# Kernel optimization log

Measured on AMD Instinct MI355X. Metric: run time of the kernel, lower is better.

The kernel has to match this reference:

```python
import jax, jax.numpy as jnp
import numpy as np

K = 16  # neighbors
EPS = 1e-3  # Keras BatchNormalization default epsilon


def _bn(x, gamma, beta, mean, var):
    return (x - mean) * jax.lax.rsqrt(var + EPS) * gamma + beta


def setup_inputs() -> dict:
    key = jax.random.key(0)
    ks = jax.random.split(key, 16)
    B, P, C = 128, 256, 64
    inp = {
        "points": jax.random.normal(ks[0], (B, P, 3), jnp.float32),
        "features": jax.random.normal(ks[1], (B, P, C), jnp.float32),
        "w0": jax.random.normal(ks[2], (2 * C, 64), jnp.float32) * 0.08,
        "w1": jax.random.normal(ks[3], (64, 64), jnp.float32) * 0.12,
        "w2": jax.random.normal(ks[4], (64, 64), jnp.float32) * 0.12,
        "gammas": 0.8 + 0.4 * jax.random.uniform(ks[5], (3, 64), jnp.float32),
        "betas": 0.1 * jax.random.normal(ks[6], (3, 64), jnp.float32),
        "means": 0.1 * jax.random.normal(ks[7], (3, 64), jnp.float32),
        "variances": 0.5 + jax.random.uniform(ks[8], (3, 64), jnp.float32),
        "sc_w": jax.random.normal(ks[9], (C, 64), jnp.float32) * 0.12,
        "sc_gamma": 0.8 + 0.4 * jax.random.uniform(ks[10], (64,), jnp.float32),
        "sc_beta": 0.1 * jax.random.normal(ks[11], (64,), jnp.float32),
        "sc_mean": 0.1 * jax.random.normal(ks[12], (64,), jnp.float32),
        "sc_var": 0.5 + jax.random.uniform(ks[13], (64,), jnp.float32),
    }
    return inp


def reference(points, features, w0, w1, w2, gammas, betas, means, variances,
              sc_w, sc_gamma, sc_beta, sc_mean, sc_var):
    B, P, C = features.shape
    # pairwise squared-distance matrix: ||a||^2 - 2 a.b + ||b||^2  -> [B, P, P]
    r = jnp.sum(points * points, axis=2, keepdims=True)  # [B, P, 1]
    m = jnp.einsum('bpc,bqc->bpq', points, points)
    d = r - 2.0 * m + jnp.swapaxes(r, 1, 2)
    # top_k of -d: K+1 nearest (incl. self at position 0), drop self
    _, idx = jax.lax.top_k(-d, K + 1)
    idx = idx[:, :, 1:]  # [B, P, K]
    # KNN gather of features
    knn_fts = features[jnp.arange(B)[:, None, None], idx]  # [B, P, K, C]
    center = jnp.broadcast_to(features[:, :, None, :], (B, P, K, C))
    x = jnp.concatenate([center, knn_fts - center], axis=-1)  # [B, P, K, 2C]
    # per-edge MLP: 1x1 conv + BN (inference) + relu
    for i, w in enumerate((w0, w1, w2)):
        x = jnp.einsum('bpkc,cd->bpkd', x, w)
        x = _bn(x, gammas[i], betas[i], means[i], variances[i])
        x = jax.nn.relu(x)
    fts = jnp.mean(x, axis=2)  # average pooling over neighbors -> [B, P, 64]
    # shortcut 1x1 conv + BN
    sc = jnp.einsum('bpc,cd->bpd', features, sc_w)
    sc = _bn(sc, sc_gamma, sc_beta, sc_mean, sc_var)
    return jax.nn.relu(sc + fts)
```

## Files before the change

kernel.cpp:

```cpp
#include <hip/hip_runtime.h>
#include <math.h>

#define NBATCH 128
#define NP 256
#define NC 64
#define KNN 16
#define EPSV 1e-3f

typedef __bf16 bf16_t;
typedef bf16_t bf16x8 __attribute__((ext_vector_type(8)));
typedef float f32x4 __attribute__((ext_vector_type(4)));
typedef unsigned short u16x4 __attribute__((ext_vector_type(4)));

static __device__ __forceinline__ f32x4 mfma16(bf16x8 a, bf16x8 b, f32x4 c) {
    return __builtin_amdgcn_mfma_f32_16x16x32_bf16(a, b, c, 0, 0, 0);
}
static __device__ __forceinline__ unsigned short f2bfu(float f) {
    union { bf16_t b; unsigned short u; } cv; cv.b = (bf16_t)f; return cv.u;
}
static __device__ __forceinline__ float bfu2f(unsigned short u) {
    unsigned x = ((unsigned)u) << 16;
    return __int_as_float((int)x);
}
static __device__ __forceinline__ unsigned umin2(unsigned a, unsigned b) { return a < b ? a : b; }
static __device__ __forceinline__ unsigned umax2(unsigned a, unsigned b) { return a > b ? a : b; }

static __device__ __forceinline__ bf16x8 packrelu(f32x4 a, f32x4 b) {
    bf16x8 r;
    r[0] = (bf16_t)fmaxf(a[0], 0.f); r[1] = (bf16_t)fmaxf(a[1], 0.f);
    r[2] = (bf16_t)fmaxf(a[2], 0.f); r[3] = (bf16_t)fmaxf(a[3], 0.f);
    r[4] = (bf16_t)fmaxf(b[0], 0.f); r[5] = (bf16_t)fmaxf(b[1], 0.f);
    r[6] = (bf16_t)fmaxf(b[2], 0.f); r[7] = (bf16_t)fmaxf(b[3], 0.f);
    return r;
}

template <int CTRL>
static __device__ __forceinline__ float dppadd(float v) {
    int x = __builtin_amdgcn_mov_dpp(__float_as_int(v), CTRL, 0xF, 0xF, true);
    return v + __int_as_float(x);
}
static __device__ __forceinline__ float sum16(float v) {
    v = dppadd<0xB1>(v);
    v = dppadd<0x4E>(v);
    v = dppadd<0x141>(v);
    v = dppadd<0x140>(v);
    return v;
}

#define CFENCE() asm volatile("" ::: "memory")

#define INSERTK(k_)                                                   \
    do {                                                              \
        _Pragma("unroll")                                             \
        for (int ii = KNN - 1; ii >= 1; --ii)                         \
            bk[ii] = umin2(umax2((k_), bk[ii - 1]), bk[ii]);          \
        bk[0] = umin2((k_), bk[0]);                                   \
    } while (0)

__global__ __launch_bounds__(256) void setup_kernel(
    const float* __restrict__ points, const float* __restrict__ features,
    const float* __restrict__ w0, const float* __restrict__ w1,
    const float* __restrict__ w2, const float* __restrict__ sc_w,
    const float* __restrict__ gammas, const float* __restrict__ betas,
    const float* __restrict__ means, const float* __restrict__ variances,
    const float* __restrict__ sc_gamma, const float* __restrict__ sc_beta,
    const float* __restrict__ sc_mean, const float* __restrict__ sc_var,
    unsigned short* __restrict__ fbf, unsigned short* __restrict__ wsf,
    float* __restrict__ bnp, int* __restrict__ knn_out)
{
    const int bid = blockIdx.x;
    if (bid < 1024) {
        const int tid = bid * 256 + threadIdx.x;
        const float4 a = ((const float4*)features)[tid * 2];
        const float4 b = ((const float4*)features)[tid * 2 + 1];
        union { unsigned short s[8]; uint4 v; } r;
        r.s[0] = f2bfu(a.x); r.s[1] = f2bfu(a.y); r.s[2] = f2bfu(a.z); r.s[3] = f2bfu(a.w);
        r.s[4] = f2bfu(b.x); r.s[5] = f2bfu(b.y); r.s[6] = f2bfu(b.z); r.s[7] = f2bfu(b.w);
        ((uint4*)fbf)[tid] = r.v;
    } else if (bid < 1106) {
        const int tid = (bid - 1024) * 256 + threadIdx.x;
        if (tid < 20480) {
            const int region = tid >> 12;
            const int e2 = tid & 4095;
            const int f = e2 >> 9;
            const int r = e2 & 511;
            const int lane = r >> 3, j = r & 7;
            const int ks = f >> 2, t = f & 3;
            const int m = lane & 15;
            const int k_in = ks * 32 + (lane >> 4) * 8 + j;
            const int kp = (t >> 1) * 32 + (m >> 2) * 8 + (t & 1) * 4 + (m & 3);
            float v;
            if (region == 0)      v = w0[k_in * 64 + kp] - w0[(64 + k_in) * 64 + kp];
            else if (region == 1) v = w0[(64 + k_in) * 64 + kp];
            else if (region == 2) {
                float s1 = gammas[k_in] * rsqrtf(variances[k_in] + EPSV);
                v = s1 * w1[k_in * 64 + kp];
            } else if (region == 3) {
                float s2 = gammas[64 + k_in] * rsqrtf(variances[64 + k_in] + EPSV);
                v = s2 * w2[k_in * 64 + kp];
            } else {
                v = sc_w[k_in * 64 + (4 * m + t)];
            }
            wsf[tid] = f2bfu(v);
        } else {
            const int e = tid - 20480;
            if (e < 192) {
                const int L = e >> 6;
                const int pos = e & 63;
                const int t = pos >> 4, m = pos & 15;
                const int c = (t >> 1) * 32 + (m >> 2) * 8 + (t & 1) * 4 + (m & 3);
                float scl = gammas[L * 64 + c] * rsqrtf(variances[L * 64 + c] + EPSV);
                float shf = betas[L * 64 + c] - means[L * 64 + c] * scl;
                bnp[e] = shf / scl;
            } else if (e < 256) {
                const int c = e - 192;
                float s3 = gammas[128 + c] * rsqrtf(variances[128 + c] + EPSV);
                bnp[e] = s3 * (1.f / 16.f);
            } else if (e < 320) {
                const int c = e - 256;
                bnp[e] = sc_gamma[c] * rsqrtf(sc_var[c] + EPSV);
            } else if (e < 384) {
                const int c = e - 320;
                float s = sc_gamma[c] * rsqrtf(sc_var[c] + EPSV);
                bnp[e] = sc_beta[c] - sc_mean[c] * s;
            }
        }
    } else {
        __shared__ __align__(16) float4 sp[NP];
        __shared__ unsigned sk[128][17];
        const int kb = bid - 1106;
        const int bb = kb >> 1;
        const int qbase = (kb & 1) * 128;
        const int t = threadIdx.x;
        const int qt = t & 127;
        const int half = t >> 7;
        const int p = qbase + qt;

        const float* pb = points + (size_t)bb * NP * 3;
        sp[t] = make_float4(pb[t * 3 + 0], pb[t * 3 + 1], pb[t * 3 + 2], 0.f);
        __syncthreads();

        const float4 qp = sp[p];
        unsigned bk[KNN];
#pragma unroll
        for (int i = 0; i < KNN; ++i) bk[i] = 0xFFFFFFFFu;

        const int cbase = half * 128;
#pragma unroll 4
        for (int c = 0; c < 128; ++c) {
            const int cand = cbase + c;
            const float4 P = sp[cand];
            const float dx = qp.x - P.x, dy = qp.y - P.y, dz = qp.z - P.z;
            const float d = fmaf(dx, dx, fmaf(dy, dy, dz * dz));
            unsigned key = (__float_as_uint(d) & 0xFFFFFF00u) | (unsigned)cand;
            key = (cand == p) ? 0xFFFFFFFFu : key;
            INSERTK(key);
        }

        if (half == 1) {
#pragma unroll
            for (int i = 0; i < KNN; ++i) sk[qt][i] = bk[i];
        }
        __syncthreads();
        if (half == 0) {
            for (int j = 0; j < KNN; ++j) {
                const unsigned key = sk[qt][j];
                if (key >= bk[KNN - 1]) break;
                INSERTK(key);
            }
            int* op = knn_out + ((size_t)bb * NP + p) * KNN;
#pragma unroll
            for (int i = 0; i < KNN; ++i) op[i] = (int)(bk[i] & 0xFFu);
        }
    }
}

__global__ __launch_bounds__(256) void edge_kernel(
    const unsigned short* __restrict__ fbf, const int* __restrict__ knn_idx,
    const unsigned short* __restrict__ wsf, const float* __restrict__ bnp,
    float* __restrict__ out)
{
    __shared__ __align__(16) float s0buf[4][8][64];
    __shared__ __align__(16) unsigned short ftsbuf[4][8][64];

    const int tid = threadIdx.x;
    const int wid = tid >> 6;
    const int l = tid & 63;
    const int i = l & 15;
    const int h = l >> 4;
    const int wg = (blockIdx.x & 7) * 128 + (blockIdx.x >> 3);
    const int p0 = (wg * 4 + wid) * 8;
    const int b = p0 >> 8;

    bf16x8 wr[24];
    {
        const bf16x8* __restrict__ W = (const bf16x8*)(wsf + 4096);
#pragma unroll
        for (int f = 0; f < 24; ++f) wr[f] = W[f * 64 + l];
    }
    #define WF(fi_) (wr[fi_])

    f32x4 cin2[4], cin3[4];
#pragma unroll
    for (int t = 0; t < 4; ++t) {
        cin2[t] = *(const f32x4*)&bnp[64 + t * 16 + 4 * h];
        cin3[t] = *(const f32x4*)&bnp[128 + t * 16 + 4 * h];
    }

    {
        const bf16x8* __restrict__ WV = (const bf16x8*)(wsf);
        const unsigned short* cp = fbf + (size_t)(p0 + (i & 7)) * NC;
        bf16x8 b0 = *(const bf16x8*)(cp + 8 * h);
        bf16x8 b1 = *(const bf16x8*)(cp + 32 + 8 * h);
#pragma unroll
        for (int t = 0; t < 4; ++t) {
            f32x4 acc = *(const f32x4*)&bnp[t * 16 + 4 * h];
            acc = mfma16(WV[t * 64 + l], b0, acc);
            acc = mfma16(WV[(4 + t) * 64 + l], b1, acc);
            if (i < 8)
                *(f32x4*)&s0buf[wid][i][t * 16 + 4 * h] = acc;
        }
    }
    int nks[8];
#pragma unroll
    for (int q = 0; q < 8; ++q) nks[q] = knn_idx[(size_t)(p0 + q) * KNN + i];
    CFENCE();

    bf16x8 fb0, fb1;
    {
        const unsigned short* sp = fbf + (size_t)(b * NP + nks[0]) * NC;
        fb0 = *(const bf16x8*)(sp + 8 * h);
        fb1 = *(const bf16x8*)(sp + 32 + 8 * h);
    }

#pragma unroll
    for (int q = 0; q < 8; ++q) {
        f32x4 acc[4];
#pragma unroll
        for (int t = 0; t < 4; ++t) {
            f32x4 z = *(const f32x4*)&s0buf[wid][q][t * 16 + 4 * h];
            z = mfma16(WF(t), fb0, z);
            acc[t] = mfma16(WF(4 + t), fb1, z);
        }
        bf16x8 g0, g1;
        if (q < 7) {
            const unsigned short* sp = fbf + (size_t)(b * NP + nks[(q + 1) & 7]) * NC;
            g0 = *(const bf16x8*)(sp + 8 * h);
            g1 = *(const bf16x8*)(sp + 32 + 8 * h);
        }
        bf16x8 x0 = packrelu(acc[0], acc[1]);
        bf16x8 x1 = packrelu(acc[2], acc[3]);

#pragma unroll
        for (int t = 0; t < 4; ++t) {
            f32x4 z = mfma16(WF(8 + t), x0, cin2[t]);
            acc[t] = mfma16(WF(12 + t), x1, z);
        }
        bf16x8 y0 = packrelu(acc[0], acc[1]);
        bf16x8 y1 = packrelu(acc[2], acc[3]);

#pragma unroll
        for (int t = 0; t < 4; ++t) {
            f32x4 z = mfma16(WF(16 + t), y0, cin3[t]);
            acc[t] = mfma16(WF(20 + t), y1, z);
        }
        float st[4][4];
#pragma unroll
        for (int t = 0; t < 4; ++t)
#pragma unroll
            for (int r = 0; r < 4; ++r)
                st[t][r] = sum16(fmaxf(acc[t][r], 0.f));
        if (i == 0) {
#pragma unroll
            for (int t = 0; t < 4; ++t) {
                u16x4 pk;
#pragma unroll
                for (int r = 0; r < 4; ++r) pk[r] = f2bfu(st[t][r]);
                *(u16x4*)&ftsbuf[wid][q][(t >> 1) * 32 + h * 8 + (t & 1) * 4] = pk;
            }
        }
        fb0 = g0; fb1 = g1;
    }
    CFENCE();

    {
        const bf16x8* __restrict__ WS = (const bf16x8*)(wsf + 16384);
        const int i4 = 4 * i;
        float4 sscl = *(const float4*)&bnp[256 + i4];
        float4 sshf = *(const float4*)&bnp[320 + i4];
        float4 f3q  = *(const float4*)&bnp[192 + i4];
        const unsigned short* fp = fbf + (size_t)(p0 + (i & 7)) * NC;
        bf16x8 a0 = *(const bf16x8*)(fp + 8 * h);
        bf16x8 a1 = *(const bf16x8*)(fp + 32 + 8 * h);
        f32x4 acc[4];
#pragma unroll
        for (int t = 0; t < 4; ++t) {
            f32x4 z = {0.f, 0.f, 0.f, 0.f};
            z = mfma16(a0, WS[t * 64 + l], z);
            acc[t] = mfma16(a1, WS[(4 + t) * 64 + l], z);
        }
        if (h < 2) {
            const float* ss_ = (const float*)&sscl;
            const float* sf_ = (const float*)&sshf;
            const float* f3_ = (const float*)&f3q;
#pragma unroll
            for (int r = 0; r < 4; ++r) {
                const int q = h * 4 + r;
                u16x4 ftsu = *(const u16x4*)&ftsbuf[wid][q][i4];
                float4 o;
                float* o_ = (float*)&o;
#pragma unroll
                for (int t = 0; t < 4; ++t)
                    o_[t] = fmaxf(fmaf(acc[t][r], ss_[t], sf_[t]) + bfu2f(ftsu[t]) * f3_[t], 0.f);
                *(float4*)&out[(size_t)(p0 + q) * NC + i4] = o;
            }
        }
    }
    #undef WF
}

extern "C" void kernel_launch(void* const* d_in, const int* in_sizes, int n_in,
                              void* d_out, int out_size, void* d_ws, size_t ws_size,
                              hipStream_t stream) {
    const float* points    = (const float*)d_in[0];
    const float* features  = (const float*)d_in[1];
    const float* w0        = (const float*)d_in[2];
    const float* w1        = (const float*)d_in[3];
    const float* w2        = (const float*)d_in[4];
    const float* gammas    = (const float*)d_in[5];
    const float* betas     = (const float*)d_in[6];
    const float* means     = (const float*)d_in[7];
    const float* variances = (const float*)d_in[8];
    const float* sc_w      = (const float*)d_in[9];
    const float* sc_gamma  = (const float*)d_in[10];
    const float* sc_beta   = (const float*)d_in[11];
    const float* sc_mean   = (const float*)d_in[12];
    const float* sc_var    = (const float*)d_in[13];
    float* out = (float*)d_out;

    int* knn_buf = (int*)d_ws;
    unsigned short* fbf = (unsigned short*)((char*)d_ws + (1 << 21));
    unsigned short* wsf = (unsigned short*)((char*)d_ws + (3 << 21));
    float* bnp = (float*)((char*)d_ws + (3 << 21) + 40960);

    setup_kernel<<<1362, 256, 0, stream>>>(points, features, w0, w1, w2, sc_w,
                                           gammas, betas, means, variances,
                                           sc_gamma, sc_beta, sc_mean, sc_var,
                                           fbf, wsf, bnp, knn_buf);
    edge_kernel<<<NBATCH * NP / 32, 256, 0, stream>>>(fbf, knn_buf, wsf, bnp, out);
}
```

Before: 50.39 us.

## Fuse KNN, feature conversion and edge MLP into one per-batch kernel

Merges the KNN search, the bf16 feature conversion and the edge MLP into a single kernel. Each block handles half a batch and stages that batch's bf16 features in swizzled LDS, so neighbour gathers read LDS instead of global memory and the knn indices and bf16 feature buffer never go to global memory. Weight and BN preparation stays in a small separate kernel. The trade-off is a grid of only 256 blocks with large LDS use (about 50KB), which lowers occupancy and parallelism. The KNN phase also keeps the same half-idle merge step as before, and each block converts all 256 rows of its batch, so every batch is converted twice.

```diff
diff --git a/kernel.cpp b/kernel.cpp
--- a/kernel.cpp
+++ b/kernel.cpp
@@ -57,94 +57,108 @@
         bk[0] = umin2((k_), bk[0]);                                   \
     } while (0)
 
-__global__ __launch_bounds__(256) void setup_kernel(
-    const float* __restrict__ points, const float* __restrict__ features,
+__global__ __launch_bounds__(256) void prep_kernel(
     const float* __restrict__ w0, const float* __restrict__ w1,
     const float* __restrict__ w2, const float* __restrict__ sc_w,
     const float* __restrict__ gammas, const float* __restrict__ betas,
     const float* __restrict__ means, const float* __restrict__ variances,
     const float* __restrict__ sc_gamma, const float* __restrict__ sc_beta,
     const float* __restrict__ sc_mean, const float* __restrict__ sc_var,
-    unsigned short* __restrict__ fbf, unsigned short* __restrict__ wsf,
-    float* __restrict__ bnp, int* __restrict__ knn_out)
+    unsigned short* __restrict__ wsf, float* __restrict__ bnp)
 {
-    const int bid = blockIdx.x;
-    if (bid < 1024) {
-        const int tid = bid * 256 + threadIdx.x;
-        const float4 a = ((const float4*)features)[tid * 2];
-        const float4 b = ((const float4*)features)[tid * 2 + 1];
-        union { unsigned short s[8]; uint4 v; } r;
-        r.s[0] = f2bfu(a.x); r.s[1] = f2bfu(a.y); r.s[2] = f2bfu(a.z); r.s[3] = f2bfu(a.w);
-        r.s[4] = f2bfu(b.x); r.s[5] = f2bfu(b.y); r.s[6] = f2bfu(b.z); r.s[7] = f2bfu(b.w);
-        ((uint4*)fbf)[tid] = r.v;
-    } else if (bid < 1106) {
-        const int tid = (bid - 1024) * 256 + threadIdx.x;
-        if (tid < 20480) {
-            const int region = tid >> 12;
-            const int e2 = tid & 4095;
-            const int f = e2 >> 9;
-            const int r = e2 & 511;
-            const int lane = r >> 3, j = r & 7;
-            const int ks = f >> 2, t = f & 3;
-            const int m = lane & 15;
-            const int k_in = ks * 32 + (lane >> 4) * 8 + j;
-            const int kp = (t >> 1) * 32 + (m >> 2) * 8 + (t & 1) * 4 + (m & 3);
-            float v;
-            if (region == 0)      v = w0[k_in * 64 + kp] - w0[(64 + k_in) * 64 + kp];
-            else if (region == 1) v = w0[(64 + k_in) * 64 + kp];
-            else if (region == 2) {
-                float s1 = gammas[k_in] * rsqrtf(variances[k_in] + EPSV);
-                v = s1 * w1[k_in * 64 + kp];
-            } else if (region == 3) {
-                float s2 = gammas[64 + k_in] * rsqrtf(variances[64 + k_in] + EPSV);
-                v = s2 * w2[k_in * 64 + kp];
-            } else {
-                v = sc_w[k_in * 64 + (4 * m + t)];
-            }
-            wsf[tid] = f2bfu(v);
+    const int tid = blockIdx.x * 256 + threadIdx.x;
+    if (tid < 20480) {
+        const int region = tid >> 12;
+        const int e2 = tid & 4095;
+        const int f = e2 >> 9;
+        const int r = e2 & 511;
+        const int lane = r >> 3, j = r & 7;
+        const int ks = f >> 2, t = f & 3;
+        const int m = lane & 15;
+        const int k_in = ks * 32 + (lane >> 4) * 8 + j;
+        const int kp = (t >> 1) * 32 + (m >> 2) * 8 + (t & 1) * 4 + (m & 3);
+        float v;
+        if (region == 0)      v = w0[k_in * 64 + kp] - w0[(64 + k_in) * 64 + kp];
+        else if (region == 1) v = w0[(64 + k_in) * 64 + kp];
+        else if (region == 2) {
+            float s1 = gammas[k_in] * rsqrtf(variances[k_in] + EPSV);
+            v = s1 * w1[k_in * 64 + kp];
+        } else if (region == 3) {
+            float s2 = gammas[64 + k_in] * rsqrtf(variances[64 + k_in] + EPSV);
+            v = s2 * w2[k_in * 64 + kp];
         } else {
-            const int e = tid - 20480;
-            if (e < 192) {
-                const int L = e >> 6;
-                const int pos = e & 63;
-                const int t = pos >> 4, m = pos & 15;
-                const int c = (t >> 1) * 32 + (m >> 2) * 8 + (t & 1) * 4 + (m & 3);
-                float scl = gammas[L * 64 + c] * rsqrtf(variances[L * 64 + c] + EPSV);
-                float shf = betas[L * 64 + c] - means[L * 64 + c] * scl;
-                bnp[e] = shf / scl;
-            } else if (e < 256) {
-                const int c = e - 192;
-                float s3 = gammas[128 + c] * rsqrtf(variances[128 + c] + EPSV);
-                bnp[e] = s3 * (1.f / 16.f);
-            } else if (e < 320) {
-                const int c = e - 256;
-                bnp[e] = sc_gamma[c] * rsqrtf(sc_var[c] + EPSV);
-            } else if (e < 384) {
-                const int c = e - 320;
-                float s = sc_gamma[c] * rsqrtf(sc_var[c] + EPSV);
-                bnp[e] = sc_beta[c] - sc_mean[c] * s;
-            }
-        }
+            v = sc_w[k_in * 64 + (4 * m + t)];
+        }
+        wsf[tid] = f2bfu(v);
     } else {
-        __shared__ __align__(16) float4 sp[NP];
-        __shared__ unsigned sk[128][17];
-        const int kb = bid - 1106;
-        const int bb = kb >> 1;
-        const int qbase = (kb & 1) * 128;
-        const int t = threadIdx.x;
+        const int e = tid - 20480;
+        if (e < 192) {
+            const int L = e >> 6;
+            const int pos = e & 63;
+            const int t = pos >> 4, m = pos & 15;
+            const int c = (t >> 1) * 32 + (m >> 2) * 8 + (t & 1) * 4 + (m & 3);
+            float scl = gammas[L * 64 + c] * rsqrtf(variances[L * 64 + c] + EPSV);
+            float shf = betas[L * 64 + c] - means[L * 64 + c] * scl;
+            bnp[e] = shf / scl;
+        } else if (e < 256) {
+            const int c = e - 192;
+            float s3 = gammas[128 + c] * rsqrtf(variances[128 + c] + EPSV);
+            bnp[e] = s3 * (1.f / 16.f);
+        } else if (e < 320) {
+            const int c = e - 256;
+            bnp[e] = sc_gamma[c] * rsqrtf(sc_var[c] + EPSV);
+        } else if (e < 384) {
+            const int c = e - 320;
+            float s = sc_gamma[c] * rsqrtf(sc_var[c] + EPSV);
+            bnp[e] = sc_beta[c] - sc_mean[c] * s;
+        }
+    }
+}
+
+__global__ __launch_bounds__(256) void mega_kernel(
+    const float* __restrict__ points, const float* __restrict__ features,
+    const unsigned short* __restrict__ wsf, const float* __restrict__ bnp,
+    float* __restrict__ out)
+{
+    __shared__ __align__(16) unsigned short fLDS[NP * NC];
+    __shared__ __align__(16) float4 sp[NP];
+    __shared__ unsigned sk[128][17];
+    __shared__ unsigned short nkbuf[128][16];
+    __shared__ __align__(16) float s0buf[4][8][64];
+    __shared__ __align__(16) unsigned short ftsbuf[4][8][64];
+
+    const int kb = blockIdx.x;
+    const int bb = kb >> 1;
+    const int qbase = (kb & 1) * 128;
+    const int t = threadIdx.x;
+
+    {
+        const float* pb = points + (size_t)bb * NP * 3;
+        sp[t] = make_float4(pb[t * 3 + 0], pb[t * 3 + 1], pb[t * 3 + 2], 0.f);
+        const float* fb = features + (size_t)bb * NP * NC;
+#pragma unroll
+        for (int cc = 0; cc < 8; ++cc) {
+            const int c = t + cc * 256;
+            const int row = c >> 3, ch8 = c & 7;
+            const float4 a = *(const float4*)&fb[row * NC + ch8 * 8];
+            const float4 b2 = *(const float4*)&fb[row * NC + ch8 * 8 + 4];
+            union { unsigned short s[8]; uint4 v; } r;
+            r.s[0] = f2bfu(a.x); r.s[1] = f2bfu(a.y); r.s[2] = f2bfu(a.z); r.s[3] = f2bfu(a.w);
+            r.s[4] = f2bfu(b2.x); r.s[5] = f2bfu(b2.y); r.s[6] = f2bfu(b2.z); r.s[7] = f2bfu(b2.w);
+            const int sc = ch8 ^ (row & 7);
+            *(uint4*)&fLDS[row * NC + sc * 8] = r.v;
+        }
+    }
+    __syncthreads();
+
+    {
         const int qt = t & 127;
         const int half = t >> 7;
         const int p = qbase + qt;
-
-        const float* pb = points + (size_t)bb * NP * 3;
-        sp[t] = make_float4(pb[t * 3 + 0], pb[t * 3 + 1], pb[t * 3 + 2], 0.f);
-        __syncthreads();
-
         const float4 qp = sp[p];
         unsigned bk[KNN];
 #pragma unroll
-        for (int i = 0; i < KNN; ++i) bk[i] = 0xFFFFFFFFu;
-
+        for (int ii = 0; ii < KNN; ++ii) bk[ii] = 0xFFFFFFFFu;
         const int cbase = half * 128;
 #pragma unroll 4
         for (int c = 0; c < 128; ++c) {
@@ -156,10 +170,9 @@
             key = (cand == p) ? 0xFFFFFFFFu : key;
             INSERTK(key);
         }
-
         if (half == 1) {
 #pragma unroll
-            for (int i = 0; i < KNN; ++i) sk[qt][i] = bk[i];
+            for (int ii = 0; ii < KNN; ++ii) sk[qt][ii] = bk[ii];
         }
         __syncthreads();
         if (half == 0) {
@@ -168,29 +181,17 @@
                 if (key >= bk[KNN - 1]) break;
                 INSERTK(key);
             }
-            int* op = knn_out + ((size_t)bb * NP + p) * KNN;
-#pragma unroll
-            for (int i = 0; i < KNN; ++i) op[i] = (int)(bk[i] & 0xFFu);
-        }
-    }
-}
-
-__global__ __launch_bounds__(256) void edge_kernel(
-    const unsigned short* __restrict__ fbf, const int* __restrict__ knn_idx,
-    const unsigned short* __restrict__ wsf, const float* __restrict__ bnp,
-    float* __restrict__ out)
-{
-    __shared__ __align__(16) float s0buf[4][8][64];
-    __shared__ __align__(16) unsigned short ftsbuf[4][8][64];
-
-    const int tid = threadIdx.x;
-    const int wid = tid >> 6;
-    const int l = tid & 63;
+#pragma unroll
+            for (int ii = 0; ii < KNN; ++ii)
+                nkbuf[qt][ii] = (unsigned short)(bk[ii] & 0xFFu);
+        }
+    }
+    __syncthreads();
+
+    const int wid = t >> 6;
+    const int l = t & 63;
     const int i = l & 15;
     const int h = l >> 4;
-    const int wg = (blockIdx.x & 7) * 128 + (blockIdx.x >> 3);
-    const int p0 = (wg * 4 + wid) * 8;
-    const int b = p0 >> 8;
 
     bf16x8 wr[24];
     {
@@ -198,125 +199,128 @@
 #pragma unroll
         for (int f = 0; f < 24; ++f) wr[f] = W[f * 64 + l];
     }
-    #define WF(fi_) (wr[fi_])
-
     f32x4 cin2[4], cin3[4];
 #pragma unroll
-    for (int t = 0; t < 4; ++t) {
-        cin2[t] = *(const f32x4*)&bnp[64 + t * 16 + 4 * h];
-        cin3[t] = *(const f32x4*)&bnp[128 + t * 16 + 4 * h];
-    }
-
-    {
-        const bf16x8* __restrict__ WV = (const bf16x8*)(wsf);
-        const unsigned short* cp = fbf + (size_t)(p0 + (i & 7)) * NC;
-        bf16x8 b0 = *(const bf16x8*)(cp + 8 * h);
-        bf16x8 b1 = *(const bf16x8*)(cp + 32 + 8 * h);
-#pragma unroll
-        for (int t = 0; t < 4; ++t) {
-            f32x4 acc = *(const f32x4*)&bnp[t * 16 + 4 * h];
-            acc = mfma16(WV[t * 64 + l], b0, acc);
-            acc = mfma16(WV[(4 + t) * 64 + l], b1, acc);
-            if (i < 8)
-                *(f32x4*)&s0buf[wid][i][t * 16 + 4 * h] = acc;
-        }
-    }
-    int nks[8];
-#pragma unroll
-    for (int q = 0; q < 8; ++q) nks[q] = knn_idx[(size_t)(p0 + q) * KNN + i];
-    CFENCE();
-
-    bf16x8 fb0, fb1;
-    {
-        const unsigned short* sp = fbf + (size_t)(b * NP + nks[0]) * NC;
-        fb0 = *(const bf16x8*)(sp + 8 * h);
-        fb1 = *(const bf16x8*)(sp + 32 + 8 * h);
-    }
-
-#pragma unroll
-    for (int q = 0; q < 8; ++q) {
-        f32x4 acc[4];
-#pragma unroll
-        for (int t = 0; t < 4; ++t) {
-            f32x4 z = *(const f32x4*)&s0buf[wid][q][t * 16 + 4 * h];
-            z = mfma16(WF(t), fb0, z);
-            acc[t] = mfma16(WF(4 + t), fb1, z);
-        }
-        bf16x8 g0, g1;
-        if (q < 7) {
-            const unsigned short* sp = fbf + (size_t)(b * NP + nks[(q + 1) & 7]) * NC;
-            g0 = *(const bf16x8*)(sp + 8 * h);
-            g1 = *(const bf16x8*)(sp + 32 + 8 * h);
-        }
-        bf16x8 x0 = packrelu(acc[0], acc[1]);
-        bf16x8 x1 = packrelu(acc[2], acc[3]);
-
-#pragma unroll
-        for (int t = 0; t < 4; ++t) {
-            f32x4 z = mfma16(WF(8 + t), x0, cin2[t]);
-            acc[t] = mfma16(WF(12 + t), x1, z);
-        }
-        bf16x8 y0 = packrelu(acc[0], acc[1]);
-        bf16x8 y1 = packrelu(acc[2], acc[3]);
-
-#pragma unroll
-        for (int t = 0; t < 4; ++t) {
-            f32x4 z = mfma16(WF(16 + t), y0, cin3[t]);
-            acc[t] = mfma16(WF(20 + t), y1, z);
-        }
-        float st[4][4];
-#pragma unroll
-        for (int t = 0; t < 4; ++t)
-#pragma unroll
-            for (int r = 0; r < 4; ++r)
-                st[t][r] = sum16(fmaxf(acc[t][r], 0.f));
-        if (i == 0) {
-#pragma unroll
-            for (int t = 0; t < 4; ++t) {
-                u16x4 pk;
-#pragma unroll
-                for (int r = 0; r < 4; ++r) pk[r] = f2bfu(st[t][r]);
-                *(u16x4*)&ftsbuf[wid][q][(t >> 1) * 32 + h * 8 + (t & 1) * 4] = pk;
-            }
-        }
-        fb0 = g0; fb1 = g1;
-    }
-    CFENCE();
-
-    {
-        const bf16x8* __restrict__ WS = (const bf16x8*)(wsf + 16384);
-        const int i4 = 4 * i;
-        float4 sscl = *(const float4*)&bnp[256 + i4];
-        float4 sshf = *(const float4*)&bnp[320 + i4];
-        float4 f3q  = *(const float4*)&bnp[192 + i4];
-        const unsigned short* fp = fbf + (size_t)(p0 + (i & 7)) * NC;
-        bf16x8 a0 = *(const bf16x8*)(fp + 8 * h);
-        bf16x8 a1 = *(const bf16x8*)(fp + 32 + 8 * h);
-        f32x4 acc[4];
-#pragma unroll
-        for (int t = 0; t < 4; ++t) {
-            f32x4 z = {0.f, 0.f, 0.f, 0.f};
-            z = mfma16(a0, WS[t * 64 + l], z);
-            acc[t] = mfma16(a1, WS[(4 + t) * 64 + l], z);
-        }
-        if (h < 2) {
-            const float* ss_ = (const float*)&sscl;
-            const float* sf_ = (const float*)&sshf;
-            const float* f3_ = (const float*)&f3q;
-#pragma unroll
-            for (int r = 0; r < 4; ++r) {
-                const int q = h * 4 + r;
-                u16x4 ftsu = *(const u16x4*)&ftsbuf[wid][q][i4];
-                float4 o;
-                float* o_ = (float*)&o;
-#pragma unroll
-                for (int t = 0; t < 4; ++t)
-                    o_[t] = fmaxf(fmaf(acc[t][r], ss_[t], sf_[t]) + bfu2f(ftsu[t]) * f3_[t], 0.f);
-                *(float4*)&out[(size_t)(p0 + q) * NC + i4] = o;
-            }
-        }
-    }
-    #undef WF
+    for (int tq = 0; tq < 4; ++tq) {
+        cin2[tq] = *(const f32x4*)&bnp[64 + tq * 16 + 4 * h];
+        cin3[tq] = *(const f32x4*)&bnp[128 + tq * 16 + 4 * h];
+    }
+
+    const bf16x8* __restrict__ WV = (const bf16x8*)(wsf);
+    const bf16x8* __restrict__ WS = (const bf16x8*)(wsf + 16384);
+
+    for (int seg = 0; seg < 4; ++seg) {
+        const int qr0 = seg * 32 + wid * 8;
+
+        {
+            const int crow = qbase + qr0 + (i & 7);
+            const int swl = crow & 7;
+            bf16x8 b0 = *(const bf16x8*)&fLDS[crow * NC + (h ^ swl) * 8];
+            bf16x8 b1 = *(const bf16x8*)&fLDS[crow * NC + ((4 + h) ^ swl) * 8];
+#pragma unroll
+            for (int tq = 0; tq < 4; ++tq) {
+                f32x4 acc = *(const f32x4*)&bnp[tq * 16 + 4 * h];
+                acc = mfma16(WV[tq * 64 + l], b0, acc);
+                acc = mfma16(WV[(4 + tq) * 64 + l], b1, acc);
+                if (i < 8)
+                    *(f32x4*)&s0buf[wid][i][tq * 16 + 4 * h] = acc;
+            }
+        }
+        int nks[8];
+#pragma unroll
+        for (int q = 0; q < 8; ++q) nks[q] = nkbuf[qr0 + q][i];
+        CFENCE();
+
+        bf16x8 fb0, fb1;
+        {
+            const int nk = nks[0], swn = nk & 7;
+            fb0 = *(const bf16x8*)&fLDS[nk * NC + (h ^ swn) * 8];
+            fb1 = *(const bf16x8*)&fLDS[nk * NC + ((4 + h) ^ swn) * 8];
+        }
+
+#pragma unroll
+        for (int q = 0; q < 8; ++q) {
+            f32x4 acc[4];
+#pragma unroll
+            for (int tq = 0; tq < 4; ++tq) {
+                f32x4 z = *(const f32x4*)&s0buf[wid][q][tq * 16 + 4 * h];
+                z = mfma16(wr[tq], fb0, z);
+                acc[tq] = mfma16(wr[4 + tq], fb1, z);
+            }
+            bf16x8 g0, g1;
+            if (q < 7) {
+                const int nk = nks[q + 1], swn = nk & 7;
+                g0 = *(const bf16x8*)&fLDS[nk * NC + (h ^ swn) * 8];
+                g1 = *(const bf16x8*)&fLDS[nk * NC + ((4 + h) ^ swn) * 8];
+            }
+            bf16x8 x0 = packrelu(acc[0], acc[1]);
+            bf16x8 x1 = packrelu(acc[2], acc[3]);
+#pragma unroll
+            for (int tq = 0; tq < 4; ++tq) {
+                f32x4 z = mfma16(wr[8 + tq], x0, cin2[tq]);
+                acc[tq] = mfma16(wr[12 + tq], x1, z);
+            }
+            bf16x8 y0 = packrelu(acc[0], acc[1]);
+            bf16x8 y1 = packrelu(acc[2], acc[3]);
+#pragma unroll
+            for (int tq = 0; tq < 4; ++tq) {
+                f32x4 z = mfma16(wr[16 + tq], y0, cin3[tq]);
+                acc[tq] = mfma16(wr[20 + tq], y1, z);
+            }
+            float st[4][4];
+#pragma unroll
+            for (int tq = 0; tq < 4; ++tq)
+#pragma unroll
+                for (int r = 0; r < 4; ++r)
+                    st[tq][r] = sum16(fmaxf(acc[tq][r], 0.f));
+            if (i == 0) {
+#pragma unroll
+                for (int tq = 0; tq < 4; ++tq) {
+                    u16x4 pk;
+#pragma unroll
+                    for (int r = 0; r < 4; ++r) pk[r] = f2bfu(st[tq][r]);
+                    *(u16x4*)&ftsbuf[wid][q][(tq >> 1) * 32 + h * 8 + (tq & 1) * 4] = pk;
+                }
+            }
+            fb0 = g0; fb1 = g1;
+        }
+        CFENCE();
+
+        {
+            const int i4 = 4 * i;
+            float4 sscl = *(const float4*)&bnp[256 + i4];
+            float4 sshf = *(const float4*)&bnp[320 + i4];
+            float4 f3q  = *(const float4*)&bnp[192 + i4];
+            const int crow = qbase + qr0 + (i & 7);
+            const int swl = crow & 7;
+            bf16x8 a0 = *(const bf16x8*)&fLDS[crow * NC + (h ^ swl) * 8];
+            bf16x8 a1 = *(const bf16x8*)&fLDS[crow * NC + ((4 + h) ^ swl) * 8];
+            f32x4 acc[4];
+#pragma unroll
+            for (int tq = 0; tq < 4; ++tq) {
+                f32x4 z = {0.f, 0.f, 0.f, 0.f};
+                z = mfma16(a0, WS[tq * 64 + l], z);
+                acc[tq] = mfma16(a1, WS[(4 + tq) * 64 + l], z);
+            }
+            if (h < 2) {
+                const float* ss_ = (const float*)&sscl;
+                const float* sf_ = (const float*)&sshf;
+                const float* f3_ = (const float*)&f3q;
+#pragma unroll
+                for (int r = 0; r < 4; ++r) {
+                    const int q = h * 4 + r;
+                    u16x4 ftsu = *(const u16x4*)&ftsbuf[wid][q][i4];
+                    float4 o;
+                    float* o_ = (float*)&o;
+#pragma unroll
+                    for (int tq = 0; tq < 4; ++tq)
+                        o_[tq] = fmaxf(fmaf(acc[tq][r], ss_[tq], sf_[tq]) + bfu2f(ftsu[tq]) * f3_[tq], 0.f);
+                    *(float4*)&out[(size_t)(bb * NP + qbase + qr0 + q) * NC + i4] = o;
+                }
+            }
+        }
+        CFENCE();
+    }
 }
 
 extern "C" void kernel_launch(void* const* d_in, const int* in_sizes, int n_in,
@@ -338,14 +342,11 @@
     const float* sc_var    = (const float*)d_in[13];
     float* out = (float*)d_out;
 
-    int* knn_buf = (int*)d_ws;
-    unsigned short* fbf = (unsigned short*)((char*)d_ws + (1 << 21));
-    unsigned short* wsf = (unsigned short*)((char*)d_ws + (3 << 21));
-    float* bnp = (float*)((char*)d_ws + (3 << 21) + 40960);
-
-    setup_kernel<<<1362, 256, 0, stream>>>(points, features, w0, w1, w2, sc_w,
-                                           gammas, betas, means, variances,
-                                           sc_gamma, sc_beta, sc_mean, sc_var,
-                                           fbf, wsf, bnp, knn_buf);
-    edge_kernel<<<NBATCH * NP / 32, 256, 0, stream>>>(fbf, knn_buf, wsf, bnp, out);
-}
+    unsigned short* wsf = (unsigned short*)d_ws;
+    float* bnp = (float*)((char*)d_ws + 40960);
+
+    prep_kernel<<<82, 256, 0, stream>>>(w0, w1, w2, sc_w, gammas, betas, means,
+                                        variances, sc_gamma, sc_beta, sc_mean,
+                                        sc_var, wsf, bnp);
+    mega_kernel<<<NBATCH * 2, 256, 0, stream>>>(points, features, wsf, bnp, out);
+}
```

Result: slower. 51.80 us (+2.8%).

## Transpose layer-3 MFMA so neighbor sum uses two cross-half shuffles

Applied to the files above, without the earlier changes.

Layer 3 now swaps the MFMA operands so the output puts the neighbor dimension across the four accumulator registers and the 16-lane halves. The neighbor pooling becomes an in-register add plus two xor-shuffles, replacing sixteen 4-step DPP reductions. Pooled features stay in fp32 in shared memory instead of bf16. The w2 and shortcut weights and the BN bias layout are reordered to match, and the center-feature loads are reused for the shortcut. The tradeoffs are scalar 4-byte output stores in place of float4 stores, and a larger shared buffer.

```diff
diff --git a/kernel.cpp b/kernel.cpp
--- a/kernel.cpp
+++ b/kernel.cpp
@@ -10,17 +10,12 @@
 typedef __bf16 bf16_t;
 typedef bf16_t bf16x8 __attribute__((ext_vector_type(8)));
 typedef float f32x4 __attribute__((ext_vector_type(4)));
-typedef unsigned short u16x4 __attribute__((ext_vector_type(4)));
 
 static __device__ __forceinline__ f32x4 mfma16(bf16x8 a, bf16x8 b, f32x4 c) {
     return __builtin_amdgcn_mfma_f32_16x16x32_bf16(a, b, c, 0, 0, 0);
 }
 static __device__ __forceinline__ unsigned short f2bfu(float f) {
     union { bf16_t b; unsigned short u; } cv; cv.b = (bf16_t)f; return cv.u;
-}
-static __device__ __forceinline__ float bfu2f(unsigned short u) {
-    unsigned x = ((unsigned)u) << 16;
-    return __int_as_float((int)x);
 }
 static __device__ __forceinline__ unsigned umin2(unsigned a, unsigned b) { return a < b ? a : b; }
 static __device__ __forceinline__ unsigned umax2(unsigned a, unsigned b) { return a > b ? a : b; }
@@ -32,19 +27,6 @@
     r[4] = (bf16_t)fmaxf(b[0], 0.f); r[5] = (bf16_t)fmaxf(b[1], 0.f);
     r[6] = (bf16_t)fmaxf(b[2], 0.f); r[7] = (bf16_t)fmaxf(b[3], 0.f);
     return r;
-}
-
-template <int CTRL>
-static __device__ __forceinline__ float dppadd(float v) {
-    int x = __builtin_amdgcn_mov_dpp(__float_as_int(v), CTRL, 0xF, 0xF, true);
-    return v + __int_as_float(x);
-}
-static __device__ __forceinline__ float sum16(float v) {
-    v = dppadd<0xB1>(v);
-    v = dppadd<0x4E>(v);
-    v = dppadd<0x141>(v);
-    v = dppadd<0x140>(v);
-    return v;
 }
 
 #define CFENCE() asm volatile("" ::: "memory")
@@ -88,29 +70,39 @@
             const int ks = f >> 2, t = f & 3;
             const int m = lane & 15;
             const int k_in = ks * 32 + (lane >> 4) * 8 + j;
-            const int kp = (t >> 1) * 32 + (m >> 2) * 8 + (t & 1) * 4 + (m & 3);
             float v;
-            if (region == 0)      v = w0[k_in * 64 + kp] - w0[(64 + k_in) * 64 + kp];
-            else if (region == 1) v = w0[(64 + k_in) * 64 + kp];
-            else if (region == 2) {
-                float s1 = gammas[k_in] * rsqrtf(variances[k_in] + EPSV);
-                v = s1 * w1[k_in * 64 + kp];
-            } else if (region == 3) {
-                float s2 = gammas[64 + k_in] * rsqrtf(variances[64 + k_in] + EPSV);
-                v = s2 * w2[k_in * 64 + kp];
+            if (region <= 2) {
+                const int kp = (t >> 1) * 32 + (m >> 2) * 8 + (t & 1) * 4 + (m & 3);
+                if (region == 0)      v = w0[k_in * 64 + kp] - w0[(64 + k_in) * 64 + kp];
+                else if (region == 1) v = w0[(64 + k_in) * 64 + kp];
+                else {
+                    float s1 = gammas[k_in] * rsqrtf(variances[k_in] + EPSV);
+                    v = s1 * w1[k_in * 64 + kp];
+                }
             } else {
-                v = sc_w[k_in * 64 + (4 * m + t)];
+                const int col = t * 16 + m;
+                if (region == 3) {
+                    float s2 = gammas[64 + k_in] * rsqrtf(variances[64 + k_in] + EPSV);
+                    v = s2 * w2[k_in * 64 + col];
+                } else {
+                    v = sc_w[k_in * 64 + col];
+                }
             }
             wsf[tid] = f2bfu(v);
         } else {
             const int e = tid - 20480;
-            if (e < 192) {
+            if (e < 128) {
                 const int L = e >> 6;
                 const int pos = e & 63;
                 const int t = pos >> 4, m = pos & 15;
                 const int c = (t >> 1) * 32 + (m >> 2) * 8 + (t & 1) * 4 + (m & 3);
                 float scl = gammas[L * 64 + c] * rsqrtf(variances[L * 64 + c] + EPSV);
                 float shf = betas[L * 64 + c] - means[L * 64 + c] * scl;
+                bnp[e] = shf / scl;
+            } else if (e < 192) {
+                const int c = e - 128;
+                float scl = gammas[128 + c] * rsqrtf(variances[128 + c] + EPSV);
+                float shf = betas[128 + c] - means[128 + c] * scl;
                 bnp[e] = shf / scl;
             } else if (e < 256) {
                 const int c = e - 192;
@@ -181,7 +173,7 @@
     float* __restrict__ out)
 {
     __shared__ __align__(16) float s0buf[4][8][64];
-    __shared__ __align__(16) unsigned short ftsbuf[4][8][64];
+    __shared__ __align__(16) float ftsbuf[4][8][64];
 
     const int tid = threadIdx.x;
     const int wid = tid >> 6;
@@ -198,25 +190,25 @@
 #pragma unroll
         for (int f = 0; f < 24; ++f) wr[f] = W[f * 64 + l];
     }
-    #define WF(fi_) (wr[fi_])
-
-    f32x4 cin2[4], cin3[4];
+    f32x4 cin2[4];
+    float c3b[4];
 #pragma unroll
     for (int t = 0; t < 4; ++t) {
         cin2[t] = *(const f32x4*)&bnp[64 + t * 16 + 4 * h];
-        cin3[t] = *(const f32x4*)&bnp[128 + t * 16 + 4 * h];
-    }
-
+        c3b[t] = bnp[128 + t * 16 + i];
+    }
+
+    bf16x8 a0, a1;
     {
+        const unsigned short* cp = fbf + (size_t)(p0 + (i & 7)) * NC;
+        a0 = *(const bf16x8*)(cp + 8 * h);
+        a1 = *(const bf16x8*)(cp + 32 + 8 * h);
         const bf16x8* __restrict__ WV = (const bf16x8*)(wsf);
-        const unsigned short* cp = fbf + (size_t)(p0 + (i & 7)) * NC;
-        bf16x8 b0 = *(const bf16x8*)(cp + 8 * h);
-        bf16x8 b1 = *(const bf16x8*)(cp + 32 + 8 * h);
 #pragma unroll
         for (int t = 0; t < 4; ++t) {
             f32x4 acc = *(const f32x4*)&bnp[t * 16 + 4 * h];
-            acc = mfma16(WV[t * 64 + l], b0, acc);
-            acc = mfma16(WV[(4 + t) * 64 + l], b1, acc);
+            acc = mfma16(WV[t * 64 + l], a0, acc);
+            acc = mfma16(WV[(4 + t) * 64 + l], a1, acc);
             if (i < 8)
                 *(f32x4*)&s0buf[wid][i][t * 16 + 4 * h] = acc;
         }
@@ -239,8 +231,8 @@
 #pragma unroll
         for (int t = 0; t < 4; ++t) {
             f32x4 z = *(const f32x4*)&s0buf[wid][q][t * 16 + 4 * h];
-            z = mfma16(WF(t), fb0, z);
-            acc[t] = mfma16(WF(4 + t), fb1, z);
+            z = mfma16(wr[t], fb0, z);
+            acc[t] = mfma16(wr[4 + t], fb1, z);
         }
         bf16x8 g0, g1;
         if (q < 7) {
@@ -253,31 +245,25 @@
 
 #pragma unroll
         for (int t = 0; t < 4; ++t) {
-            f32x4 z = mfma16(WF(8 + t), x0, cin2[t]);
-            acc[t] = mfma16(WF(12 + t), x1, z);
+            f32x4 z = mfma16(wr[8 + t], x0, cin2[t]);
+            acc[t] = mfma16(wr[12 + t], x1, z);
         }
         bf16x8 y0 = packrelu(acc[0], acc[1]);
         bf16x8 y1 = packrelu(acc[2], acc[3]);
 
 #pragma unroll
         for (int t = 0; t < 4; ++t) {
-            f32x4 z = mfma16(WF(16 + t), y0, cin3[t]);
-            acc[t] = mfma16(WF(20 + t), y1, z);
-        }
-        float st[4][4];
-#pragma unroll
-        for (int t = 0; t < 4; ++t)
-#pragma unroll
-            for (int r = 0; r < 4; ++r)
-                st[t][r] = sum16(fmaxf(acc[t][r], 0.f));
-        if (i == 0) {
-#pragma unroll
-            for (int t = 0; t < 4; ++t) {
-                u16x4 pk;
-#pragma unroll
-                for (int r = 0; r < 4; ++r) pk[r] = f2bfu(st[t][r]);
-                *(u16x4*)&ftsbuf[wid][q][(t >> 1) * 32 + h * 8 + (t & 1) * 4] = pk;
-            }
+            f32x4 z = {c3b[t], c3b[t], c3b[t], c3b[t]};
+            z = mfma16(y0, wr[16 + t], z);
+            acc[t] = mfma16(y1, wr[20 + t], z);
+        }
+#pragma unroll
+        for (int t = 0; t < 4; ++t) {
+            float s = fmaxf(acc[t][0], 0.f) + fmaxf(acc[t][1], 0.f)
+                    + fmaxf(acc[t][2], 0.f) + fmaxf(acc[t][3], 0.f);
+            s += __shfl_xor(s, 16, 64);
+            s += __shfl_xor(s, 32, 64);
+            if (h == 0) ftsbuf[wid][q][t * 16 + i] = s;
         }
         fb0 = g0; fb1 = g1;
     }
@@ -285,13 +271,13 @@
 
     {
         const bf16x8* __restrict__ WS = (const bf16x8*)(wsf + 16384);
-        const int i4 = 4 * i;
-        float4 sscl = *(const float4*)&bnp[256 + i4];
-        float4 sshf = *(const float4*)&bnp[320 + i4];
-        float4 f3q  = *(const float4*)&bnp[192 + i4];
-        const unsigned short* fp = fbf + (size_t)(p0 + (i & 7)) * NC;
-        bf16x8 a0 = *(const bf16x8*)(fp + 8 * h);
-        bf16x8 a1 = *(const bf16x8*)(fp + 32 + 8 * h);
+        float sscl[4], sshf[4], f3[4];
+#pragma unroll
+        for (int t = 0; t < 4; ++t) {
+            sscl[t] = bnp[256 + t * 16 + i];
+            sshf[t] = bnp[320 + t * 16 + i];
+            f3[t]   = bnp[192 + t * 16 + i];
+        }
         f32x4 acc[4];
 #pragma unroll
         for (int t = 0; t < 4; ++t) {
@@ -300,23 +286,18 @@
             acc[t] = mfma16(a1, WS[(4 + t) * 64 + l], z);
         }
         if (h < 2) {
-            const float* ss_ = (const float*)&sscl;
-            const float* sf_ = (const float*)&sshf;
-            const float* f3_ = (const float*)&f3q;
 #pragma unroll
             for (int r = 0; r < 4; ++r) {
                 const int q = h * 4 + r;
-                u16x4 ftsu = *(const u16x4*)&ftsbuf[wid][q][i4];
-                float4 o;
-                float* o_ = (float*)&o;
-#pragma unroll
-                for (int t = 0; t < 4; ++t)
-                    o_[t] = fmaxf(fmaf(acc[t][r], ss_[t], sf_[t]) + bfu2f(ftsu[t]) * f3_[t], 0.f);
-                *(float4*)&out[(size_t)(p0 + q) * NC + i4] = o;
+                float* op = out + (size_t)(p0 + q) * NC;
+#pragma unroll
+                for (int t = 0; t < 4; ++t) {
+                    float fts = ftsbuf[wid][q][t * 16 + i];
+                    op[t * 16 + i] = fmaxf(fmaf(acc[t][r], sscl[t], sshf[t]) + fts * f3[t], 0.f);
+                }
             }
         }
     }
-    #undef WF
 }
 
 extern "C" void kernel_launch(void* const* d_in, const int* in_sizes, int n_in,
```

New measurement: 48.02 us. -4.7%, faster.
